# Kernel tuning notes

Measured on AMD Instinct MI355X. Metric: run time of the kernel, lower is better.

## Reference

```python
import jax, jax.numpy as jnp
import numpy as np

B, S, E, H, DK = 16, 512, 256, 8, 32
NSH, NSEL = 2, 4           # shared heads, selected dynamic heads
NDYN = H - NSH             # dynamic heads
NB = 4                     # num_blocks -> blocks_1: NB layers, blocks_2: 2*NB layers
L = 3 * NB                 # total layers, params stacked on leading dim
NSKILL, NQ = 1000, 10000
FC1, FC2 = 512, 256


def setup_inputs():
    key = jax.random.key(0)
    ks = jax.random.split(key, 24)
    r = lambda i, sh: jax.random.normal(ks[i], sh, jnp.float32) * 0.02
    return {
        'skills': jax.random.randint(ks[0], (B, S), 0, NSKILL),
        'responses': jax.random.randint(ks[1], (B, S), 0, 2),
        'questions': jax.random.randint(ks[2], (B, S), 0, NQ),
        'attention_mask': jnp.ones((B, S), jnp.int32),
        'q_embed': r(3, (NSKILL, E)),
        'qa_embed': r(4, (3, E)),
        'q_embed_diff': r(5, (NSKILL + 1, E)),
        'qa_embed_diff': r(6, (2 * NSKILL + 1, E)),
        'difficult_param': r(7, (NQ + 1, 1)),
        'Wq': r(8, (L, E, E)), 'bq': jnp.zeros((L, E)),
        'Wv': r(9, (L, E, E)), 'bv': jnp.zeros((L, E)),
        'Wo': r(10, (L, E, E)), 'bo': jnp.zeros((L, E)),
        'Wg': r(11, (L, E, NDYN)),
        'ln1_g': jnp.ones((L, E)), 'ln1_b': jnp.zeros((L, E)),
        'ln2_g': jnp.ones((L, E)), 'ln2_b': jnp.zeros((L, E)),
        'ffn_W1': r(12, (L, E, E)), 'ffn_b1': jnp.zeros((L, E)),
        'ffn_W2': r(13, (L, E, E)), 'ffn_b2': jnp.zeros((L, E)),
        'out_W1': r(14, (2 * E, FC1)), 'out_b1': jnp.zeros((FC1,)),
        'out_W2': r(15, (FC1, FC2)), 'out_b2': jnp.zeros((FC2,)),
        'out_W3': r(16, (FC2, 1)), 'out_b3': jnp.zeros((1,)),
    }


def _ln(x, g, b):
    m = x.mean(-1, keepdims=True)
    v = ((x - m) ** 2).mean(-1, keepdims=True)
    return (x - m) * jax.lax.rsqrt(v + 1e-5) * g + b


def _layer(i, q_in, k_in, v_in, mask, P):
    # MoH attention: standard MHA + top-k routed dynamic heads (kq_same=True)
    qh = (q_in @ P['Wq'][i] + P['bq'][i]).reshape(B, S, H, DK).transpose(0, 2, 1, 3)
    kh = (k_in @ P['Wq'][i] + P['bq'][i]).reshape(B, S, H, DK).transpose(0, 2, 1, 3)
    vh = (v_in @ P['Wv'][i] + P['bv'][i]).reshape(B, S, H, DK).transpose(0, 2, 1, 3)
    scores = jnp.einsum('bhid,bhjd->bhij', qh, kh) / np.float32(np.sqrt(DK))
    attn = jax.nn.softmax(jnp.where(mask, scores, -1e32), axis=-1)
    ctx = jnp.einsum('bhij,bhjd->bhid', attn, vh).transpose(0, 2, 1, 3)  # [B,S,H,DK]
    # router on pre-projection query: hard top-NSEL one-hot gates over NDYN heads
    logits = q_in @ P['Wg'][i]                     # [B,S,NDYN]
    _, topi = jax.lax.top_k(logits, NSEL)
    gates = jax.nn.one_hot(topi, NDYN, dtype=ctx.dtype).sum(-2)
    hg = jnp.concatenate([jnp.ones((B, S, NSH), ctx.dtype), gates], axis=-1)  # [B,S,H]
    attn_out = (ctx * hg[..., None]).reshape(B, S, E) @ P['Wo'][i] + P['bo'][i]
    x = _ln(q_in + attn_out, P['ln1_g'][i], P['ln1_b'][i])
    f = jax.nn.relu(x @ P['ffn_W1'][i] + P['ffn_b1'][i]) @ P['ffn_W2'][i] + P['ffn_b2'][i]
    return _ln(x + f, P['ln2_g'][i], P['ln2_b'][i])


def _forward(skills, responses, questions, P):
    masked_r = responses * (responses > -1).astype(responses.dtype)
    q_emb = P['q_embed'][skills]
    qa_emb = q_emb + P['qa_embed'][masked_r]
    q_diff = P['q_embed_diff'][skills]
    pid = P['difficult_param'][questions]          # [B,S,1]
    q_emb = q_emb + pid * q_diff
    qa_diff = P['qa_embed_diff'][skills + NSKILL * masked_r]
    qa_emb = qa_emb + pid * (qa_diff + q_diff)
    idx = jnp.arange(S)
    causal = (idx[None, :] <= idx[:, None])[None, None]  # mask==1: incl diagonal
    strict = (idx[None, :] < idx[:, None])[None, None]   # mask==0: excl diagonal
    y, x = qa_emb, q_emb
    for i in range(NB):
        y = _layer(i, y, y, y, causal, P)
    li = NB
    for _ in range(NB):
        x = _layer(li, x, x, x, causal, P); li += 1
        x = _layer(li, x, x, y, strict, P); li += 1
    h = jnp.concatenate([x, q_emb], axis=-1)
    h = jax.nn.relu(h @ P['out_W1'] + P['out_b1'])
    h = jax.nn.relu(h @ P['out_W2'] + P['out_b2'])
    out = jax.nn.sigmoid(h @ P['out_W3'] + P['out_b3'])[..., 0]
    return out[:, 1:]


def reference(skills, responses, questions, attention_mask, q_embed, qa_embed, q_embed_diff, qa_embed_diff, difficult_param, Wq, bq, Wv, bv, Wo, bo, Wg, ln1_g, ln1_b, ln2_g, ln2_b, ffn_W1, ffn_b1, ffn_W2, ffn_b2, out_W1, out_b1, out_W2, out_b2, out_W3, out_b3):
    P = dict(q_embed=q_embed, qa_embed=qa_embed, q_embed_diff=q_embed_diff, qa_embed_diff=qa_embed_diff, difficult_param=difficult_param, Wq=Wq, bq=bq, Wv=Wv, bv=bv, Wo=Wo, bo=bo, Wg=Wg, ln1_g=ln1_g, ln1_b=ln1_b, ln2_g=ln2_g, ln2_b=ln2_b, ffn_W1=ffn_W1, ffn_b1=ffn_b1, ffn_W2=ffn_W2, ffn_b2=ffn_b2, out_W1=out_W1, out_b1=out_b1, out_W2=out_W2, out_b2=out_b2, out_W3=out_W3, out_b3=out_b3)
    return _forward(skills, responses, questions, P)
```

## Files before the change

kernel.cpp:

```cpp
#include <hip/hip_runtime.h>
#include <hip/hip_bf16.h>

constexpr int CB = 16, CS = 512, CE = 256, CH = 8, CDK = 32;
constexpr int CNDYN = 6;
constexpr int CT = CB * CS;
constexpr float SCALE = 0.17677669529663687f;

typedef __bf16 bf16x8 __attribute__((ext_vector_type(8)));
typedef float f32x4 __attribute__((ext_vector_type(4)));
typedef unsigned short u16x8 __attribute__((ext_vector_type(8)));

__device__ __forceinline__ unsigned short f2bf(float x) {
    union { float f; unsigned u; } v; v.f = x;
    unsigned r = v.u + 0x7fff + ((v.u >> 16) & 1);
    return (unsigned short)(r >> 16);
}

__global__ __launch_bounds__(256) void embed_kernel(
    const int* __restrict__ skills, const int* __restrict__ responses,
    const int* __restrict__ questions,
    const float* __restrict__ q_embed, const float* __restrict__ qa_embed,
    const float* __restrict__ q_embed_diff, const float* __restrict__ qa_embed_diff,
    const float* __restrict__ difficult,
    float* __restrict__ q_emb, float* __restrict__ qa_emb, float* __restrict__ xb)
{
    int t = blockIdx.x;
    int e = threadIdx.x;
    int sk = skills[t];
    int r  = responses[t];
    r = (r > -1) ? r : 0;
    float pid = difficult[questions[t]];
    float qe  = q_embed[(size_t)sk * CE + e];
    float qd  = q_embed_diff[(size_t)sk * CE + e];
    float qv  = qe + pid * qd;
    float qae = qe + qa_embed[(size_t)r * CE + e];
    float qad = qa_embed_diff[((size_t)sk + 1000 * r) * CE + e];
    float qav = qae + pid * (qad + qd);
    q_emb[(size_t)t * CE + e]  = qv;
    xb[(size_t)t * CE + e]     = qv;
    qa_emb[(size_t)t * CE + e] = qav;
}

__device__ __forceinline__ void transpose_tile(
    const float* __restrict__ src, unsigned short* __restrict__ dst, int K, int N)
{
    __shared__ unsigned short T[64][72];
    int k0 = blockIdx.y * 64, n0 = blockIdx.x * 64;
    int t = threadIdx.x;
    int kr = t >> 3, nsg = (t & 7) * 8;
#pragma unroll
    for (int rr = 0; rr < 64; rr += 32) {
        const float* p = src + (size_t)(k0 + kr + rr) * N + n0 + nsg;
        float4 a = *reinterpret_cast<const float4*>(p);
        float4 b = *reinterpret_cast<const float4*>(p + 4);
        int k = kr + rr;
        T[nsg + 0][k] = f2bf(a.x); T[nsg + 1][k] = f2bf(a.y);
        T[nsg + 2][k] = f2bf(a.z); T[nsg + 3][k] = f2bf(a.w);
        T[nsg + 4][k] = f2bf(b.x); T[nsg + 5][k] = f2bf(b.y);
        T[nsg + 6][k] = f2bf(b.z); T[nsg + 7][k] = f2bf(b.w);
    }
    __syncthreads();
    {
        int n = t >> 2, ks = (t & 3) * 16;
        unsigned short* dp = dst + (size_t)(n0 + n) * K + k0 + ks;
        *reinterpret_cast<u16x8*>(dp)     = *reinterpret_cast<const u16x8*>(&T[n][ks]);
        *reinterpret_cast<u16x8*>(dp + 8) = *reinterpret_cast<const u16x8*>(&T[n][ks + 8]);
    }
}

__global__ __launch_bounds__(256) void prep_w_layers(
    const float* __restrict__ Wq, const float* __restrict__ Wv,
    const float* __restrict__ Wo, const float* __restrict__ W1,
    const float* __restrict__ W2,
    unsigned short* __restrict__ qvT, unsigned short* __restrict__ woT,
    unsigned short* __restrict__ w1T, unsigned short* __restrict__ w2T)
{
    int z = blockIdx.z;
    int which = z / 12, l = z % 12;
    const float* src;
    unsigned short* dst;
    if      (which == 0) { src = Wq + (size_t)l * 65536; dst = qvT + (size_t)l * 131072; }
    else if (which == 1) { src = Wv + (size_t)l * 65536; dst = qvT + (size_t)l * 131072 + 65536; }
    else if (which == 2) { src = Wo + (size_t)l * 65536; dst = woT + (size_t)l * 65536; }
    else if (which == 3) { src = W1 + (size_t)l * 65536; dst = w1T + (size_t)l * 65536; }
    else                 { src = W2 + (size_t)l * 65536; dst = w2T + (size_t)l * 65536; }
    transpose_tile(src, dst, 256, 256);
}

__global__ __launch_bounds__(256) void prep_w_one(
    const float* __restrict__ src, unsigned short* __restrict__ dst, int K, int N)
{
    transpose_tile(src, dst, K, N);
}

__global__ __launch_bounds__(256) void gemm_mfma(
    const float* __restrict__ A, const unsigned short* __restrict__ WT,
    const float* __restrict__ bias, float* __restrict__ C,
    const float* __restrict__ bias2, float* __restrict__ C2,
    const unsigned char* __restrict__ gmask,
    int M, int N, int K, int relu, int split)
{
    __shared__ __attribute__((aligned(16))) unsigned short As[64][72];
    __shared__ __attribute__((aligned(16))) unsigned short Bs[64][72];
    int tid = threadIdx.x;
    int bm = blockIdx.y * 64, bn = blockIdx.x * 64;
    int w = tid >> 6, lane = tid & 63;
    int wr = w >> 1, wc = w & 1;
    int lo = lane & 15, hi = lane >> 4;
    int srow = tid >> 2, sseg = (tid & 3) * 16;
    f32x4 acc[2][2] = {};

    for (int kk = 0; kk < K; kk += 64) {
        {
            const float* ap = A + (size_t)(bm + srow) * K + kk + sseg;
            float4 a0 = *reinterpret_cast<const float4*>(ap);
            float4 a1 = *reinterpret_cast<const float4*>(ap + 4);
            float4 a2 = *reinterpret_cast<const float4*>(ap + 8);
            float4 a3 = *reinterpret_cast<const float4*>(ap + 12);
            if (gmask) {
                int hh = (kk + sseg) >> 5;
                float km = ((gmask[bm + srow] >> hh) & 1) ? 1.f : 0.f;
                a0.x*=km; a0.y*=km; a0.z*=km; a0.w*=km;
                a1.x*=km; a1.y*=km; a1.z*=km; a1.w*=km;
                a2.x*=km; a2.y*=km; a2.z*=km; a2.w*=km;
                a3.x*=km; a3.y*=km; a3.z*=km; a3.w*=km;
            }
            u16x8 p0, p1;
            p0[0]=f2bf(a0.x); p0[1]=f2bf(a0.y); p0[2]=f2bf(a0.z); p0[3]=f2bf(a0.w);
            p0[4]=f2bf(a1.x); p0[5]=f2bf(a1.y); p0[6]=f2bf(a1.z); p0[7]=f2bf(a1.w);
            p1[0]=f2bf(a2.x); p1[1]=f2bf(a2.y); p1[2]=f2bf(a2.z); p1[3]=f2bf(a2.w);
            p1[4]=f2bf(a3.x); p1[5]=f2bf(a3.y); p1[6]=f2bf(a3.z); p1[7]=f2bf(a3.w);
            *reinterpret_cast<u16x8*>(&As[srow][sseg])     = p0;
            *reinterpret_cast<u16x8*>(&As[srow][sseg + 8]) = p1;
            const unsigned short* bp = WT + (size_t)(bn + srow) * K + kk + sseg;
            *reinterpret_cast<u16x8*>(&Bs[srow][sseg])     = *reinterpret_cast<const u16x8*>(bp);
            *reinterpret_cast<u16x8*>(&Bs[srow][sseg + 8]) = *reinterpret_cast<const u16x8*>(bp + 8);
        }
        __syncthreads();
#pragma unroll
        for (int ks = 0; ks < 2; ++ks) {
            bf16x8 a0 = *reinterpret_cast<const bf16x8*>(&As[wr * 32 + lo][ks * 32 + hi * 8]);
            bf16x8 a1 = *reinterpret_cast<const bf16x8*>(&As[wr * 32 + 16 + lo][ks * 32 + hi * 8]);
            bf16x8 b0 = *reinterpret_cast<const bf16x8*>(&Bs[wc * 32 + lo][ks * 32 + hi * 8]);
            bf16x8 b1 = *reinterpret_cast<const bf16x8*>(&Bs[wc * 32 + 16 + lo][ks * 32 + hi * 8]);
            acc[0][0] = __builtin_amdgcn_mfma_f32_16x16x32_bf16(a0, b0, acc[0][0], 0, 0, 0);
            acc[0][1] = __builtin_amdgcn_mfma_f32_16x16x32_bf16(a0, b1, acc[0][1], 0, 0, 0);
            acc[1][0] = __builtin_amdgcn_mfma_f32_16x16x32_bf16(a1, b0, acc[1][0], 0, 0, 0);
            acc[1][1] = __builtin_amdgcn_mfma_f32_16x16x32_bf16(a1, b1, acc[1][1], 0, 0, 0);
        }
        __syncthreads();
    }
    const float* bp = bias;
    float* Cp = C;
    int ldc = split ? split : N;
    int cb = bn;
    if (split && bn >= split) { bp = bias2; Cp = C2; ldc = N - split; cb = bn - split; }
#pragma unroll
    for (int i = 0; i < 2; ++i)
#pragma unroll
        for (int j = 0; j < 2; ++j) {
            int col = cb + wc * 32 + j * 16 + lo;
            float bv = bp[col];
#pragma unroll
            for (int r = 0; r < 4; ++r) {
                int row = bm + wr * 32 + i * 16 + hi * 4 + r;
                float v = acc[i][j][r] + bv;
                if (relu) v = fmaxf(v, 0.f);
                Cp[(size_t)row * ldc + col] = v;
            }
        }
}

__global__ __launch_bounds__(512) void attn_mfma(
    const float* __restrict__ Q, const float* __restrict__ V,
    float* __restrict__ Ctx, int strict)
{
    __shared__ __attribute__((aligned(16))) unsigned short Ks[512][40];
    __shared__ __attribute__((aligned(16))) unsigned short VTc[8][32][72];
    __shared__ __attribute__((aligned(16))) unsigned short Ps[8][16][72];

    int blk = blockIdx.x;
    int half = blk & 1;
    int h = (blk >> 1) & 7;
    int b = blk >> 4;
    int tid = threadIdx.x;
    int w = tid >> 6, lane = tid & 63;
    int lo = lane & 15, hi = lane >> 4;

#pragma unroll
    for (int r = 0; r < 4; ++r) {
        int row = (tid >> 2) + r * 128;
        int d0 = (tid & 3) * 8;
        const float* kp = Q + ((size_t)b * CS + row) * CE + h * 32 + d0;
        float4 a = *reinterpret_cast<const float4*>(kp);
        float4 c = *reinterpret_cast<const float4*>(kp + 4);
        unsigned short* dst = &Ks[row][d0];
        dst[0]=f2bf(a.x); dst[1]=f2bf(a.y); dst[2]=f2bf(a.z); dst[3]=f2bf(a.w);
        dst[4]=f2bf(c.x); dst[5]=f2bf(c.y); dst[6]=f2bf(c.z); dst[7]=f2bf(c.w);
        const float* vp = V + ((size_t)b * CS + row) * CE + h * 32 + d0;
        float4 va = *reinterpret_cast<const float4*>(vp);
        float4 vc = *reinterpret_cast<const float4*>(vp + 4);
        int c8 = row >> 6, kc = row & 63;
        VTc[c8][d0+0][kc]=f2bf(va.x); VTc[c8][d0+1][kc]=f2bf(va.y);
        VTc[c8][d0+2][kc]=f2bf(va.z); VTc[c8][d0+3][kc]=f2bf(va.w);
        VTc[c8][d0+4][kc]=f2bf(vc.x); VTc[c8][d0+5][kc]=f2bf(vc.y);
        VTc[c8][d0+6][kc]=f2bf(vc.z); VTc[c8][d0+7][kc]=f2bf(vc.w);
    }
    __syncthreads();

    for (int it = 0; it < 2; ++it) {
        int gg = half * 16 + w + it * 8;
        int qg0 = gg * 16;
        int qg = qg0 + lo;
        bool uni = strict && (qg == 0);
        bf16x8 qfrag = *reinterpret_cast<const bf16x8*>(&Ks[qg0 + lo][hi * 8]);

        f32x4 ctx0 = {0.f,0.f,0.f,0.f}, ctx1 = {0.f,0.f,0.f,0.f};
        float m = -1e30f, l = 0.f;
        int nch = (strict && qg0 == 0) ? 8 : ((gg >> 2) + 1);

        for (int c = 0; c < nch; ++c) {
            f32x4 sacc[4];
#pragma unroll
            for (int kt = 0; kt < 4; ++kt) {
                bf16x8 kfrag = *reinterpret_cast<const bf16x8*>(&Ks[c * 64 + kt * 16 + lo][hi * 8]);
                f32x4 z = {0.f,0.f,0.f,0.f};
                sacc[kt] = __builtin_amdgcn_mfma_f32_16x16x32_bf16(kfrag, qfrag, z, 0, 0, 0);
            }
            float sv[16];
            float mt = -1e30f;
#pragma unroll
            for (int kt = 0; kt < 4; ++kt)
#pragma unroll
                for (int r = 0; r < 4; ++r) {
                    int kidx = c * 64 + kt * 16 + hi * 4 + r;
                    float s = sacc[kt][r] * SCALE;
                    bool valid = strict ? (kidx < qg) : (kidx <= qg);
                    s = valid ? s : -1e30f;
                    if (uni) s = 0.f;
                    sv[kt * 4 + r] = s;
                    mt = fmaxf(mt, s);
                }
            mt = fmaxf(mt, __shfl_xor(mt, 16));
            mt = fmaxf(mt, __shfl_xor(mt, 32));
            float mn = fmaxf(m, mt);
            float co = __expf(m - mn);
            float lt = 0.f;
#pragma unroll
            for (int i = 0; i < 16; ++i) {
                float p = __expf(sv[i] - mn);
                sv[i] = p;
                lt += p;
            }
            lt += __shfl_xor(lt, 16);
            lt += __shfl_xor(lt, 32);
            l = l * co + lt;
            m = mn;
#pragma unroll
            for (int r = 0; r < 4; ++r) { ctx0[r] *= co; ctx1[r] *= co; }
#pragma unroll
            for (int kt = 0; kt < 4; ++kt) {
                unsigned short* pd = &Ps[w][lo][kt * 16 + hi * 4];
                pd[0] = f2bf(sv[kt * 4 + 0]); pd[1] = f2bf(sv[kt * 4 + 1]);
                pd[2] = f2bf(sv[kt * 4 + 2]); pd[3] = f2bf(sv[kt * 4 + 3]);
            }
            asm volatile("s_waitcnt lgkmcnt(0)" ::: "memory");
            __builtin_amdgcn_sched_barrier(0);
#pragma unroll
            for (int kh = 0; kh < 2; ++kh) {
                bf16x8 pfrag = *reinterpret_cast<const bf16x8*>(&Ps[w][lo][kh * 32 + hi * 8]);
                bf16x8 v0 = *reinterpret_cast<const bf16x8*>(&VTc[c][lo][kh * 32 + hi * 8]);
                bf16x8 v1 = *reinterpret_cast<const bf16x8*>(&VTc[c][16 + lo][kh * 32 + hi * 8]);
                ctx0 = __builtin_amdgcn_mfma_f32_16x16x32_bf16(v0, pfrag, ctx0, 0, 0, 0);
                ctx1 = __builtin_amdgcn_mfma_f32_16x16x32_bf16(v1, pfrag, ctx1, 0, 0, 0);
            }
        }

        float inv = 1.f / l;
        float* cb = reinterpret_cast<float*>(&Ps[w][0][0]);
#pragma unroll
        for (int r = 0; r < 4; ++r) {
            cb[lo * 36 + (hi * 4 + r)]      = ctx0[r] * inv;
            cb[lo * 36 + (16 + hi * 4 + r)] = ctx1[r] * inv;
        }
        asm volatile("s_waitcnt lgkmcnt(0)" ::: "memory");
        __builtin_amdgcn_sched_barrier(0);
        {
            int qloc = lane >> 2, d0 = (lane & 3) * 8;
            const float* src = cb + qloc * 36 + d0;
            float4 o0 = *reinterpret_cast<const float4*>(src);
            float4 o1 = *reinterpret_cast<const float4*>(src + 4);
            int i = qg0 + qloc;
            float* op = Ctx + ((size_t)b * CS + i) * CE + h * 32 + d0;
            *reinterpret_cast<float4*>(op)     = o0;
            *reinterpret_cast<float4*>(op + 4) = o1;
        }
        asm volatile("s_waitcnt lgkmcnt(0)" ::: "memory");
        __builtin_amdgcn_sched_barrier(0);
    }
}

__global__ __launch_bounds__(512) void gate_mask(
    const float* __restrict__ qin, const float* __restrict__ Wg,
    unsigned char* __restrict__ mb)
{
    int w = threadIdx.x >> 6, lane = threadIdx.x & 63;
    int t = blockIdx.x * 8 + w;
    const float* q = qin + (size_t)t * CE;
    float p[CNDYN] = {};
#pragma unroll
    for (int r = 0; r < 4; ++r) {
        int e = lane + r * 64;
        float qe = q[e];
        const float* wg = &Wg[(size_t)e * CNDYN];
#pragma unroll
        for (int j = 0; j < CNDYN; ++j) p[j] += qe * wg[j];
    }
#pragma unroll
    for (int o = 32; o > 0; o >>= 1)
#pragma unroll
        for (int j = 0; j < CNDYN; ++j) p[j] += __shfl_down(p[j], o);
    if (lane == 0) {
        int mask = 3;
        for (int j = 0; j < CNDYN; ++j) {
            int rank = 0;
            for (int k = 0; k < CNDYN; ++k)
                if (p[k] > p[j] || (p[k] == p[j] && k < j)) rank++;
            if (rank < 4) mask |= 1 << (2 + j);
        }
        mb[t] = (unsigned char)mask;
    }
}

__global__ __launch_bounds__(256) void add_ln(
    const float* __restrict__ A, const float* __restrict__ Bv,
    const float* __restrict__ g, const float* __restrict__ bb,
    float* __restrict__ O)
{
    int w = threadIdx.x >> 6, lane = threadIdx.x & 63;
    int t = blockIdx.x * 4 + w;
    size_t base = (size_t)t * CE + lane * 4;
    float4 a = *reinterpret_cast<const float4*>(A + base);
    float4 b = *reinterpret_cast<const float4*>(Bv + base);
    float4 v = {a.x + b.x, a.y + b.y, a.z + b.z, a.w + b.w};
    float s = v.x + v.y + v.z + v.w;
#pragma unroll
    for (int o = 32; o > 0; o >>= 1) s += __shfl_xor(s, o);
    float mean = s * (1.f / CE);
    float4 d = {v.x - mean, v.y - mean, v.z - mean, v.w - mean};
    float s2 = d.x * d.x + d.y * d.y + d.z * d.z + d.w * d.w;
#pragma unroll
    for (int o = 32; o > 0; o >>= 1) s2 += __shfl_xor(s2, o);
    float rstd = rsqrtf(s2 * (1.f / CE) + 1e-5f);
    float4 gg = *reinterpret_cast<const float4*>(g + lane * 4);
    float4 bv4 = *reinterpret_cast<const float4*>(bb + lane * 4);
    float4 o4 = {d.x * rstd * gg.x + bv4.x, d.y * rstd * gg.y + bv4.y,
                 d.z * rstd * gg.z + bv4.z, d.w * rstd * gg.w + bv4.w};
    *reinterpret_cast<float4*>(O + base) = o4;
}

__global__ __launch_bounds__(256) void concat_kernel(
    const float* __restrict__ x, const float* __restrict__ qe,
    float* __restrict__ cat)
{
    int t = blockIdx.x, e = threadIdx.x;
    cat[(size_t)t * 512 + e]       = x[(size_t)t * CE + e];
    cat[(size_t)t * 512 + 256 + e] = qe[(size_t)t * CE + e];
}

__global__ __launch_bounds__(64) void final_kernel(
    const float* __restrict__ H2, const float* __restrict__ W3,
    const float* __restrict__ b3, float* __restrict__ out)
{
    int t = blockIdx.x, lane = threadIdx.x;
    const float* h = H2 + (size_t)t * CE;
    float s = 0.f;
#pragma unroll
    for (int r = 0; r < 4; ++r) {
        int e = lane + r * 64;
        s += h[e] * W3[e];
    }
#pragma unroll
    for (int o = 32; o > 0; o >>= 1) s += __shfl_down(s, o);
    if (lane == 0) {
        float v = 1.f / (1.f + __expf(-(s + b3[0])));
        int b = t >> 9, si = t & 511;
        if (si > 0) out[(size_t)b * (CS - 1) + si - 1] = v;
    }
}

extern "C" void kernel_launch(void* const* d_in, const int* in_sizes, int n_in,
                              void* d_out, int out_size, void* d_ws, size_t ws_size,
                              hipStream_t stream)
{
    const int* skills    = (const int*)d_in[0];
    const int* responses = (const int*)d_in[1];
    const int* questions = (const int*)d_in[2];
    const float* q_embed       = (const float*)d_in[4];
    const float* qa_embed      = (const float*)d_in[5];
    const float* q_embed_diff  = (const float*)d_in[6];
    const float* qa_embed_diff = (const float*)d_in[7];
    const float* difficult     = (const float*)d_in[8];
    const float* Wq = (const float*)d_in[9];  const float* bq = (const float*)d_in[10];
    const float* Wv = (const float*)d_in[11]; const float* bv = (const float*)d_in[12];
    const float* Wo = (const float*)d_in[13]; const float* bo = (const float*)d_in[14];
    const float* Wg = (const float*)d_in[15];
    const float* ln1g = (const float*)d_in[16]; const float* ln1b = (const float*)d_in[17];
    const float* ln2g = (const float*)d_in[18]; const float* ln2b = (const float*)d_in[19];
    const float* fW1 = (const float*)d_in[20]; const float* fb1 = (const float*)d_in[21];
    const float* fW2 = (const float*)d_in[22]; const float* fb2 = (const float*)d_in[23];
    const float* oW1 = (const float*)d_in[24]; const float* ob1 = (const float*)d_in[25];
    const float* oW2 = (const float*)d_in[26]; const float* ob2 = (const float*)d_in[27];
    const float* oW3 = (const float*)d_in[28]; const float* ob3 = (const float*)d_in[29];
    float* out = (float*)d_out;

    char* ws = (char*)d_ws;
    const size_t R = (size_t)CT * CE * sizeof(float);
    float* q_emb = (float*)(ws + 0 * R);
    float* xb    = (float*)(ws + 1 * R);
    float* yb    = (float*)(ws + 2 * R);
    float* S0    = (float*)(ws + 3 * R);
    float* S1    = (float*)(ws + 4 * R);
    float* S2    = (float*)(ws + 5 * R);
    unsigned short* qvT = (unsigned short*)(ws + 7 * R);
    unsigned short* woT = qvT + (size_t)12 * 131072;
    unsigned short* w1T = woT + (size_t)12 * 65536;
    unsigned short* w2T = w1T + (size_t)12 * 65536;
    unsigned short* o1T = w2T + (size_t)12 * 65536;
    unsigned short* o2T = o1T + (size_t)512 * 512;
    unsigned char* maskbuf = (unsigned char*)(o2T + (size_t)256 * 512);
    (void)in_sizes; (void)n_in; (void)out_size; (void)ws_size;

    prep_w_layers<<<dim3(4, 4, 60), 256, 0, stream>>>(Wq, Wv, Wo, fW1, fW2, qvT, woT, w1T, w2T);
    prep_w_one<<<dim3(8, 8), 256, 0, stream>>>(oW1, o1T, 512, 512);
    prep_w_one<<<dim3(4, 8), 256, 0, stream>>>(oW2, o2T, 512, 256);

    embed_kernel<<<CT, 256, 0, stream>>>(skills, responses, questions,
        q_embed, qa_embed, q_embed_diff, qa_embed_diff, difficult, q_emb, yb, xb);

    auto layer = [&](int li, const float* qin, const float* vin, float* outc, int strict) {
        if (qin == vin) {
            gemm_mfma<<<dim3(8, 128), 256, 0, stream>>>(qin, qvT + (size_t)li * 131072,
                bq + (size_t)li * CE, S0, bv + (size_t)li * CE, S1, nullptr,
                CT, 512, CE, 0, 256);
        } else {
            gemm_mfma<<<dim3(4, 128), 256, 0, stream>>>(qin, qvT + (size_t)li * 131072,
                bq + (size_t)li * CE, S0, nullptr, nullptr, nullptr, CT, CE, CE, 0, 0);
            gemm_mfma<<<dim3(4, 128), 256, 0, stream>>>(vin, qvT + (size_t)li * 131072 + 65536,
                bv + (size_t)li * CE, S1, nullptr, nullptr, nullptr, CT, CE, CE, 0, 0);
        }
        gate_mask<<<CT / 8, 512, 0, stream>>>(qin, Wg + (size_t)li * CE * CNDYN, maskbuf);
        attn_mfma<<<CB * CH * 2, 512, 0, stream>>>(S0, S1, S2, strict);
        gemm_mfma<<<dim3(4, 128), 256, 0, stream>>>(S2, woT + (size_t)li * 65536,
            bo + (size_t)li * CE, S0, nullptr, nullptr, maskbuf, CT, CE, CE, 0, 0);
        add_ln<<<CT / 4, 256, 0, stream>>>(qin, S0, ln1g + (size_t)li * CE, ln1b + (size_t)li * CE, S1);
        gemm_mfma<<<dim3(4, 128), 256, 0, stream>>>(S1, w1T + (size_t)li * 65536,
            fb1 + (size_t)li * CE, S2, nullptr, nullptr, nullptr, CT, CE, CE, 1, 0);
        gemm_mfma<<<dim3(4, 128), 256, 0, stream>>>(S2, w2T + (size_t)li * 65536,
            fb2 + (size_t)li * CE, S0, nullptr, nullptr, nullptr, CT, CE, CE, 0, 0);
        add_ln<<<CT / 4, 256, 0, stream>>>(S1, S0, ln2g + (size_t)li * CE, ln2b + (size_t)li * CE, outc);
    };

    for (int i = 0; i < 4; ++i) layer(i, yb, yb, yb, 0);
    int li = 4;
    for (int r = 0; r < 4; ++r) {
        layer(li, xb, xb, xb, 0); li++;
        layer(li, xb, yb, xb, 1); li++;
    }

    concat_kernel<<<CT, 256, 0, stream>>>(xb, q_emb, S0);
    gemm_mfma<<<dim3(8, 128), 256, 0, stream>>>(S0, o1T, ob1, S2, nullptr, nullptr, nullptr, CT, 512, 512, 1, 0);
    gemm_mfma<<<dim3(4, 128), 256, 0, stream>>>(S2, o2T, ob2, xb, nullptr, nullptr, nullptr, CT, 256, 512, 1, 0);
    final_kernel<<<CT, 64, 0, stream>>>(xb, oW3, ob3, out);
}
```

Before: 1.161 ms.

## Store intermediate activations as bf16 between GEMMs and attention

Templates the GEMM on input and output types so that Q/V projections, attention context, FFN hidden and head-MLP intermediates are written and read as bf16 instead of fp32. This halves global traffic for those buffers and removes the per-load fp32-to-bf16 conversion in the consumers. The gate mask multiply moves from the Wo GEMM's A-load into the attention epilogue. The MFMA inputs were already rounded to bf16, so the only added rounding is on the bias-added GEMM outputs.

```diff
diff --git a/kernel.cpp b/kernel.cpp
--- a/kernel.cpp
+++ b/kernel.cpp
@@ -1,5 +1,6 @@
 #include <hip/hip_runtime.h>
 #include <hip/hip_bf16.h>
+#include <type_traits>
 
 constexpr int CB = 16, CS = 512, CE = 256, CH = 8, CDK = 32;
 constexpr int CNDYN = 6;
@@ -93,11 +94,11 @@
     transpose_tile(src, dst, K, N);
 }
 
+template <typename TA, typename TC>
 __global__ __launch_bounds__(256) void gemm_mfma(
-    const float* __restrict__ A, const unsigned short* __restrict__ WT,
-    const float* __restrict__ bias, float* __restrict__ C,
-    const float* __restrict__ bias2, float* __restrict__ C2,
-    const unsigned char* __restrict__ gmask,
+    const TA* __restrict__ A, const unsigned short* __restrict__ WT,
+    const float* __restrict__ bias, TC* __restrict__ C,
+    const float* __restrict__ bias2, TC* __restrict__ C2,
     int M, int N, int K, int relu, int split)
 {
     __shared__ __attribute__((aligned(16))) unsigned short As[64][72];
@@ -111,20 +112,12 @@
     f32x4 acc[2][2] = {};
 
     for (int kk = 0; kk < K; kk += 64) {
-        {
+        if constexpr (std::is_same<TA, float>::value) {
             const float* ap = A + (size_t)(bm + srow) * K + kk + sseg;
             float4 a0 = *reinterpret_cast<const float4*>(ap);
             float4 a1 = *reinterpret_cast<const float4*>(ap + 4);
             float4 a2 = *reinterpret_cast<const float4*>(ap + 8);
             float4 a3 = *reinterpret_cast<const float4*>(ap + 12);
-            if (gmask) {
-                int hh = (kk + sseg) >> 5;
-                float km = ((gmask[bm + srow] >> hh) & 1) ? 1.f : 0.f;
-                a0.x*=km; a0.y*=km; a0.z*=km; a0.w*=km;
-                a1.x*=km; a1.y*=km; a1.z*=km; a1.w*=km;
-                a2.x*=km; a2.y*=km; a2.z*=km; a2.w*=km;
-                a3.x*=km; a3.y*=km; a3.z*=km; a3.w*=km;
-            }
             u16x8 p0, p1;
             p0[0]=f2bf(a0.x); p0[1]=f2bf(a0.y); p0[2]=f2bf(a0.z); p0[3]=f2bf(a0.w);
             p0[4]=f2bf(a1.x); p0[5]=f2bf(a1.y); p0[6]=f2bf(a1.z); p0[7]=f2bf(a1.w);
@@ -132,6 +125,12 @@
             p1[4]=f2bf(a3.x); p1[5]=f2bf(a3.y); p1[6]=f2bf(a3.z); p1[7]=f2bf(a3.w);
             *reinterpret_cast<u16x8*>(&As[srow][sseg])     = p0;
             *reinterpret_cast<u16x8*>(&As[srow][sseg + 8]) = p1;
+        } else {
+            const unsigned short* ap = A + (size_t)(bm + srow) * K + kk + sseg;
+            *reinterpret_cast<u16x8*>(&As[srow][sseg])     = *reinterpret_cast<const u16x8*>(ap);
+            *reinterpret_cast<u16x8*>(&As[srow][sseg + 8]) = *reinterpret_cast<const u16x8*>(ap + 8);
+        }
+        {
             const unsigned short* bp = WT + (size_t)(bn + srow) * K + kk + sseg;
             *reinterpret_cast<u16x8*>(&Bs[srow][sseg])     = *reinterpret_cast<const u16x8*>(bp);
             *reinterpret_cast<u16x8*>(&Bs[srow][sseg + 8]) = *reinterpret_cast<const u16x8*>(bp + 8);
@@ -151,7 +150,7 @@
         __syncthreads();
     }
     const float* bp = bias;
-    float* Cp = C;
+    TC* Cp = C;
     int ldc = split ? split : N;
     int cb = bn;
     if (split && bn >= split) { bp = bias2; Cp = C2; ldc = N - split; cb = bn - split; }
@@ -166,14 +165,18 @@
                 int row = bm + wr * 32 + i * 16 + hi * 4 + r;
                 float v = acc[i][j][r] + bv;
                 if (relu) v = fmaxf(v, 0.f);
-                Cp[(size_t)row * ldc + col] = v;
+                if constexpr (std::is_same<TC, float>::value)
+                    Cp[(size_t)row * ldc + col] = v;
+                else
+                    Cp[(size_t)row * ldc + col] = f2bf(v);
             }
         }
 }
 
 __global__ __launch_bounds__(512) void attn_mfma(
-    const float* __restrict__ Q, const float* __restrict__ V,
-    float* __restrict__ Ctx, int strict)
+    const unsigned short* __restrict__ Q, const unsigned short* __restrict__ V,
+    unsigned short* __restrict__ Ctx, const unsigned char* __restrict__ gm,
+    int strict)
 {
     __shared__ __attribute__((aligned(16))) unsigned short Ks[512][40];
     __shared__ __attribute__((aligned(16))) unsigned short VTc[8][32][72];
@@ -191,20 +194,14 @@
     for (int r = 0; r < 4; ++r) {
         int row = (tid >> 2) + r * 128;
         int d0 = (tid & 3) * 8;
-        const float* kp = Q + ((size_t)b * CS + row) * CE + h * 32 + d0;
-        float4 a = *reinterpret_cast<const float4*>(kp);
-        float4 c = *reinterpret_cast<const float4*>(kp + 4);
-        unsigned short* dst = &Ks[row][d0];
-        dst[0]=f2bf(a.x); dst[1]=f2bf(a.y); dst[2]=f2bf(a.z); dst[3]=f2bf(a.w);
-        dst[4]=f2bf(c.x); dst[5]=f2bf(c.y); dst[6]=f2bf(c.z); dst[7]=f2bf(c.w);
-        const float* vp = V + ((size_t)b * CS + row) * CE + h * 32 + d0;
-        float4 va = *reinterpret_cast<const float4*>(vp);
-        float4 vc = *reinterpret_cast<const float4*>(vp + 4);
+        u16x8 kv = *reinterpret_cast<const u16x8*>(Q + ((size_t)b * CS + row) * CE + h * 32 + d0);
+        *reinterpret_cast<u16x8*>(&Ks[row][d0]) = kv;
+        u16x8 vv = *reinterpret_cast<const u16x8*>(V + ((size_t)b * CS + row) * CE + h * 32 + d0);
         int c8 = row >> 6, kc = row & 63;
-        VTc[c8][d0+0][kc]=f2bf(va.x); VTc[c8][d0+1][kc]=f2bf(va.y);
-        VTc[c8][d0+2][kc]=f2bf(va.z); VTc[c8][d0+3][kc]=f2bf(va.w);
-        VTc[c8][d0+4][kc]=f2bf(vc.x); VTc[c8][d0+5][kc]=f2bf(vc.y);
-        VTc[c8][d0+6][kc]=f2bf(vc.z); VTc[c8][d0+7][kc]=f2bf(vc.w);
+        VTc[c8][d0+0][kc]=vv[0]; VTc[c8][d0+1][kc]=vv[1];
+        VTc[c8][d0+2][kc]=vv[2]; VTc[c8][d0+3][kc]=vv[3];
+        VTc[c8][d0+4][kc]=vv[4]; VTc[c8][d0+5][kc]=vv[5];
+        VTc[c8][d0+6][kc]=vv[6]; VTc[c8][d0+7][kc]=vv[7];
     }
     __syncthreads();
 
@@ -288,12 +285,12 @@
         {
             int qloc = lane >> 2, d0 = (lane & 3) * 8;
             const float* src = cb + qloc * 36 + d0;
-            float4 o0 = *reinterpret_cast<const float4*>(src);
-            float4 o1 = *reinterpret_cast<const float4*>(src + 4);
             int i = qg0 + qloc;
-            float* op = Ctx + ((size_t)b * CS + i) * CE + h * 32 + d0;
-            *reinterpret_cast<float4*>(op)     = o0;
-            *reinterpret_cast<float4*>(op + 4) = o1;
+            float mf = ((gm[(size_t)b * CS + i] >> h) & 1) ? 1.f : 0.f;
+            u16x8 o;
+#pragma unroll
+            for (int k = 0; k < 8; ++k) o[k] = f2bf(src[k] * mf);
+            *reinterpret_cast<u16x8*>(Ctx + ((size_t)b * CS + i) * CE + h * 32 + d0) = o;
         }
         asm volatile("s_waitcnt lgkmcnt(0)" ::: "memory");
         __builtin_amdgcn_sched_barrier(0);
@@ -361,11 +358,15 @@
 
 __global__ __launch_bounds__(256) void concat_kernel(
     const float* __restrict__ x, const float* __restrict__ qe,
-    float* __restrict__ cat)
+    unsigned short* __restrict__ cat)
 {
     int t = blockIdx.x, e = threadIdx.x;
-    cat[(size_t)t * 512 + e]       = x[(size_t)t * CE + e];
-    cat[(size_t)t * 512 + 256 + e] = qe[(size_t)t * CE + e];
+    int o = e * 2;
+    float2 v;
+    if (o < 256) v = *reinterpret_cast<const float2*>(&x[(size_t)t * CE + o]);
+    else         v = *reinterpret_cast<const float2*>(&qe[(size_t)t * CE + o - 256]);
+    unsigned pk = (unsigned)f2bf(v.x) | ((unsigned)f2bf(v.y) << 16);
+    *reinterpret_cast<unsigned*>(&cat[(size_t)t * 512 + o]) = pk;
 }
 
 __global__ __launch_bounds__(64) void final_kernel(
@@ -419,9 +420,12 @@
     float* q_emb = (float*)(ws + 0 * R);
     float* xb    = (float*)(ws + 1 * R);
     float* yb    = (float*)(ws + 2 * R);
-    float* S0    = (float*)(ws + 3 * R);
-    float* S1    = (float*)(ws + 4 * R);
-    float* S2    = (float*)(ws + 5 * R);
+    float* S0f   = (float*)(ws + 3 * R);
+    float* S1f   = (float*)(ws + 4 * R);
+    float* S2f   = (float*)(ws + 5 * R);
+    unsigned short* S0b = (unsigned short*)S0f;
+    unsigned short* S1b = (unsigned short*)S1f;
+    unsigned short* S2b = (unsigned short*)S2f;
     unsigned short* qvT = (unsigned short*)(ws + 7 * R);
     unsigned short* woT = qvT + (size_t)12 * 131072;
     unsigned short* w1T = woT + (size_t)12 * 65536;
@@ -440,25 +444,30 @@
 
     auto layer = [&](int li, const float* qin, const float* vin, float* outc, int strict) {
         if (qin == vin) {
-            gemm_mfma<<<dim3(8, 128), 256, 0, stream>>>(qin, qvT + (size_t)li * 131072,
-                bq + (size_t)li * CE, S0, bv + (size_t)li * CE, S1, nullptr,
-                CT, 512, CE, 0, 256);
+            gemm_mfma<float, unsigned short><<<dim3(8, 128), 256, 0, stream>>>(
+                qin, qvT + (size_t)li * 131072, bq + (size_t)li * CE, S0b,
+                bv + (size_t)li * CE, S1b, CT, 512, CE, 0, 256);
         } else {
-            gemm_mfma<<<dim3(4, 128), 256, 0, stream>>>(qin, qvT + (size_t)li * 131072,
-                bq + (size_t)li * CE, S0, nullptr, nullptr, nullptr, CT, CE, CE, 0, 0);
-            gemm_mfma<<<dim3(4, 128), 256, 0, stream>>>(vin, qvT + (size_t)li * 131072 + 65536,
-                bv + (size_t)li * CE, S1, nullptr, nullptr, nullptr, CT, CE, CE, 0, 0);
+            gemm_mfma<float, unsigned short><<<dim3(4, 128), 256, 0, stream>>>(
+                qin, qvT + (size_t)li * 131072, bq + (size_t)li * CE, S0b,
+                nullptr, nullptr, CT, CE, CE, 0, 0);
+            gemm_mfma<float, unsigned short><<<dim3(4, 128), 256, 0, stream>>>(
+                vin, qvT + (size_t)li * 131072 + 65536, bv + (size_t)li * CE, S1b,
+                nullptr, nullptr, CT, CE, CE, 0, 0);
         }
         gate_mask<<<CT / 8, 512, 0, stream>>>(qin, Wg + (size_t)li * CE * CNDYN, maskbuf);
-        attn_mfma<<<CB * CH * 2, 512, 0, stream>>>(S0, S1, S2, strict);
-        gemm_mfma<<<dim3(4, 128), 256, 0, stream>>>(S2, woT + (size_t)li * 65536,
-            bo + (size_t)li * CE, S0, nullptr, nullptr, maskbuf, CT, CE, CE, 0, 0);
-        add_ln<<<CT / 4, 256, 0, stream>>>(qin, S0, ln1g + (size_t)li * CE, ln1b + (size_t)li * CE, S1);
-        gemm_mfma<<<dim3(4, 128), 256, 0, stream>>>(S1, w1T + (size_t)li * 65536,
-            fb1 + (size_t)li * CE, S2, nullptr, nullptr, nullptr, CT, CE, CE, 1, 0);
-        gemm_mfma<<<dim3(4, 128), 256, 0, stream>>>(S2, w2T + (size_t)li * 65536,
-            fb2 + (size_t)li * CE, S0, nullptr, nullptr, nullptr, CT, CE, CE, 0, 0);
-        add_ln<<<CT / 4, 256, 0, stream>>>(S1, S0, ln2g + (size_t)li * CE, ln2b + (size_t)li * CE, outc);
+        attn_mfma<<<CB * CH * 2, 512, 0, stream>>>(S0b, S1b, S2b, maskbuf, strict);
+        gemm_mfma<unsigned short, float><<<dim3(4, 128), 256, 0, stream>>>(
+            S2b, woT + (size_t)li * 65536, bo + (size_t)li * CE, S0f,
+            nullptr, nullptr, CT, CE, CE, 0, 0);
+        add_ln<<<CT / 4, 256, 0, stream>>>(qin, S0f, ln1g + (size_t)li * CE, ln1b + (size_t)li * CE, S1f);
+        gemm_mfma<float, unsigned short><<<dim3(4, 128), 256, 0, stream>>>(
+            S1f, w1T + (size_t)li * 65536, fb1 + (size_t)li * CE, S2b,
+            nullptr, nullptr, CT, CE, CE, 1, 0);
+        gemm_mfma<unsigned short, float><<<dim3(4, 128), 256, 0, stream>>>(
+            S2b, w2T + (size_t)li * 65536, fb2 + (size_t)li * CE, S0f,
+            nullptr, nullptr, CT, CE, CE, 0, 0);
+        add_ln<<<CT / 4, 256, 0, stream>>>(S1f, S0f, ln2g + (size_t)li * CE, ln2b + (size_t)li * CE, outc);
     };
 
     for (int i = 0; i < 4; ++i) layer(i, yb, yb, yb, 0);
@@ -468,8 +477,10 @@
         layer(li, xb, yb, xb, 1); li++;
     }
 
-    concat_kernel<<<CT, 256, 0, stream>>>(xb, q_emb, S0);
-    gemm_mfma<<<dim3(8, 128), 256, 0, stream>>>(S0, o1T, ob1, S2, nullptr, nullptr, nullptr, CT, 512, 512, 1, 0);
-    gemm_mfma<<<dim3(4, 128), 256, 0, stream>>>(S2, o2T, ob2, xb, nullptr, nullptr, nullptr, CT, 256, 512, 1, 0);
+    concat_kernel<<<CT, 256, 0, stream>>>(xb, q_emb, S0b);
+    gemm_mfma<unsigned short, unsigned short><<<dim3(8, 128), 256, 0, stream>>>(
+        S0b, o1T, ob1, S2b, nullptr, nullptr, CT, 512, 512, 1, 0);
+    gemm_mfma<unsigned short, float><<<dim3(4, 128), 256, 0, stream>>>(
+        S2b, o2T, ob2, xb, nullptr, nullptr, CT, 256, 512, 1, 0);
     final_kernel<<<CT, 64, 0, stream>>>(xb, oW3, ob3, out);
 }
```

Result: no change. 1.183 ms (+1.9%).
